# Kernel tuning notes

Hardware: AMD Instinct MI355X
Metric: run time of the kernel (lower is better)

Reference implementation:

```python
import jax, jax.numpy as jnp
import numpy as np

# RoIAlign 2D config (matches init_kwargs)
OUT_H, OUT_W = 7, 7
SPATIAL_SCALE = 0.25
S = 2  # sampling_ratio: S x S sample points per output bin
N, C, H, W = 4, 256, 200, 200
R = 512


def setup_inputs() -> dict:
    key = jax.random.key(0)
    k1, k2, k3, k4, k5 = jax.random.split(key, 5)
    features = jax.random.normal(k1, (N, C, H, W), dtype=jnp.float32)
    # rois in image coordinates (image is H/scale = 800 px): (batch_idx, x1, y1, x2, y2)
    img = H / SPATIAL_SCALE
    b = jax.random.randint(k2, (R,), 0, N).astype(jnp.float32)
    xy1 = jax.random.uniform(k3, (R, 2), dtype=jnp.float32, maxval=img - 96.0)
    wh = jax.random.uniform(k4, (R, 2), dtype=jnp.float32, minval=16.0, maxval=96.0)
    rois = jnp.concatenate([b[:, None], xy1, xy1 + wh], axis=1)  # [R,5]
    return {"features": features, "rois": rois}


def _axis_weights(start, bin_size, out_size, limit):
    """Per-axis sample coords -> (low/high indices [R,out*S,2], lerp weights [R,out*S,2]).
    Matches mmdet/torchvision RoIAlign CUDA kernel semantics."""
    # sample coordinate: start + (i + 0.5) * bin / S  ==  start + ph*bin + (iy+0.5)*bin/S
    i = (jnp.arange(out_size * S, dtype=jnp.float32) + 0.5) / S
    y = start[:, None] + i[None, :] * bin_size[:, None]          # [R, out*S]
    valid = (y >= -1.0) & (y <= limit)                            # kernel: skip if y<-1 or y>H
    yc = jnp.clip(y, 0.0, limit - 1.0)
    yl = jnp.floor(yc).astype(jnp.int32)                          # in [0, H-1]
    yh = jnp.minimum(yl + 1, limit - 1)
    l = yc - yl.astype(jnp.float32)                               # 0 at the top edge, as in kernel
    w = jnp.stack([1.0 - l, l], axis=-1) * valid[..., None].astype(jnp.float32)  # [R,out*S,2]
    idx = jnp.stack([yl, yh], axis=-1)                            # [R,out*S,2]
    return idx, w


def reference(features, rois):
    # order=1 (bilinear) path of RoIAlign2DFunction
    b = rois[:, 0].astype(jnp.int32)                              # [R]
    x1, y1, x2, y2 = (rois[:, k] * SPATIAL_SCALE for k in (1, 2, 3, 4))
    roi_w = jnp.maximum(x2 - x1, 1.0)
    roi_h = jnp.maximum(y2 - y1, 1.0)
    bin_w = roi_w / OUT_W
    bin_h = roi_h / OUT_H

    yidx, wy = _axis_weights(y1, bin_h, OUT_H, H)                 # [R,Hs,2]
    xidx, wx = _axis_weights(x1, bin_w, OUT_W, W)                 # [R,Ws,2]

    nhwc = jnp.transpose(features, (0, 2, 3, 1))                  # [N,H,W,C]
    # gather 2x2 bilinear neighbors for every sample point: [R,Hs,Ws,2,2,C]
    vals = nhwc[b[:, None, None, None, None],
                yidx[:, :, None, :, None],
                xidx[:, None, :, None, :]]
    samples = jnp.einsum('rhwabc,rha,rwb->rhwc', vals, wy, wx)    # [R,Hs,Ws,C]
    Hs, Ws = OUT_H * S, OUT_W * S
    pooled = samples.reshape(R, OUT_H, S, OUT_W, S, C).mean(axis=(2, 4))  # avg over S*S points
    return jnp.transpose(pooled, (0, 3, 1, 2))                    # [R,C,out_h,out_w]
```

## Files before the change

### kernel.cpp

```cpp
#include <hip/hip_runtime.h>


#define OH 7
#define OW 7
#define NSAMP 14
#define NB 4
#define CH 256
#define FH 200
#define FW 200
#define NR 512
#define CCH 16
#define NCHUNK (CH / CCH)
#define PAD 17
#define MAXF 27
#define BLK 256

__global__ __launch_bounds__(BLK) void roialign_fwd(
    const float* __restrict__ feat,
    const float* __restrict__ rois,
    float* __restrict__ out)
{
    __shared__ float tile[MAXF * MAXF * PAD];
    __shared__ int   s_il[2][NSAMP];
    __shared__ int   s_ih[2][NSAMP];
    __shared__ float s_w0[2][NSAMP];
    __shared__ float s_w1[2][NSAMP];

    const int block = blockIdx.x;
    const int r     = block >> 4;
    const int chunk = block & (NCHUNK - 1);
    const int c0    = chunk * CCH;
    const int tid   = threadIdx.x;

    const int   b  = (int)rois[r * 5 + 0];
    const float x1 = rois[r * 5 + 1] * 0.25f;
    const float y1 = rois[r * 5 + 2] * 0.25f;
    const float x2 = rois[r * 5 + 3] * 0.25f;
    const float y2 = rois[r * 5 + 4] * 0.25f;
    const float roi_w = fmaxf(x2 - x1, 1.0f);
    const float roi_h = fmaxf(y2 - y1, 1.0f);
    const float bw = roi_w * (1.0f / OW);
    const float bh = roi_h * (1.0f / OH);

    if (tid < 2 * NSAMP) {
        const int axis = tid >= NSAMP;
        const int i    = tid - axis * NSAMP;
        const float start = axis ? x1 : y1;
        const float bsz   = axis ? bw : bh;
        const float pos   = start + (i + 0.5f) * 0.5f * bsz;
        const float valid = (pos >= -1.0f && pos <= 200.0f) ? 1.0f : 0.0f;
        const float pc    = fminf(fmaxf(pos, 0.0f), 199.0f);
        const int   il    = (int)floorf(pc);
        const int   ih    = min(il + 1, 199);
        const float l     = pc - (float)il;
        s_il[axis][i] = il;
        s_ih[axis][i] = ih;
        s_w0[axis][i] = (1.0f - l) * valid;
        s_w1[axis][i] = l * valid;
    }
    __syncthreads();

    const int ylo = s_il[0][0];
    const int xlo = s_il[1][0];
    int fh = s_ih[0][NSAMP - 1] - ylo + 1;
    int fw = s_ih[1][NSAMP - 1] - xlo + 1;
    fh = min(fh, MAXF);
    fw = min(fw, MAXF);

    {
        const int tx = tid & 31;
        const int ty = tid >> 5;
        const float* fbase =
            feat + ((size_t)(b * CH + c0) * FH + ylo) * FW + xlo;
        for (int y = ty; y < fh; y += BLK / 32) {
            for (int x = tx; x < fw; x += 32) {
                const float* g = fbase + y * FW + x;
                float* l = tile + (y * fw + x) * PAD;
                #pragma unroll
                for (int c = 0; c < CCH; c++) {
                    l[c] = g[(size_t)c * (FH * FW)];
                }
            }
        }
    }
    __syncthreads();

    const int cl   = tid & (CCH - 1);
    const int slot = tid >> 4;
    const float* tc = tile + cl;

    for (int bin = slot; bin < OH * OW; bin += BLK / CCH) {
        const int ph = bin / OW;
        const int pw = bin - ph * OW;
        float acc = 0.0f;
        #pragma unroll
        for (int sy = 0; sy < 2; sy++) {
            const int gy = ph * 2 + sy;
            const int rowl = (s_il[0][gy] - ylo) * fw;
            const int rowh = (s_ih[0][gy] - ylo) * fw;
            const float wy0 = s_w0[0][gy];
            const float wy1 = s_w1[0][gy];
            #pragma unroll
            for (int sx = 0; sx < 2; sx++) {
                const int gx = pw * 2 + sx;
                const int ixl = s_il[1][gx] - xlo;
                const int ixh = s_ih[1][gx] - xlo;
                const float wx0 = s_w0[1][gx];
                const float wx1 = s_w1[1][gx];
                const float v00 = tc[(rowl + ixl) * PAD];
                const float v01 = tc[(rowl + ixh) * PAD];
                const float v10 = tc[(rowh + ixl) * PAD];
                const float v11 = tc[(rowh + ixh) * PAD];
                acc += wy0 * (wx0 * v00 + wx1 * v01)
                     + wy1 * (wx0 * v10 + wx1 * v11);
            }
        }
        out[(size_t)(r * CH + c0 + cl) * (OH * OW) + bin] = acc * 0.25f;
    }
}

extern "C" void kernel_launch(void* const* d_in, const int* in_sizes, int n_in,
                              void* d_out, int out_size, void* d_ws, size_t ws_size,
                              hipStream_t stream) {
    const float* feat = (const float*)d_in[0];
    const float* rois = (const float*)d_in[1];
    float* out = (float*)d_out;
    roialign_fwd<<<NR * NCHUNK, BLK, 0, stream>>>(feat, rois, out);
}
```

Baseline: 251.5 us.

## Switch shared tile to channel-planar layout and halve channel chunk size

Changes the shared-memory tile from a pixel-major layout with padded channel interleave to one plane per channel. It halves the channels per block from 16 to 8, so there are twice as many blocks and each uses less LDS, which should raise occupancy. The load now assigns 16-lane groups to rows of a single channel, so global reads are contiguous along x. The risk is more total blocks and redundant ROI setup per block, and MAXF is lowered to 26, which may clip large ROIs.

```diff
diff --git a/kernel.cpp b/kernel.cpp
--- a/kernel.cpp
+++ b/kernel.cpp
@@ -4,15 +4,14 @@
 #define OH 7
 #define OW 7
 #define NSAMP 14
-#define NB 4
 #define CH 256
 #define FH 200
 #define FW 200
 #define NR 512
-#define CCH 16
+#define CCH 8
 #define NCHUNK (CH / CCH)
-#define PAD 17
-#define MAXF 27
+#define MAXF 26
+#define FPAD (MAXF * MAXF)
 #define BLK 256
 
 __global__ __launch_bounds__(BLK) void roialign_fwd(
@@ -20,14 +19,14 @@
     const float* __restrict__ rois,
     float* __restrict__ out)
 {
-    __shared__ float tile[MAXF * MAXF * PAD];
+    __shared__ float tile[CCH * FPAD];
     __shared__ int   s_il[2][NSAMP];
     __shared__ int   s_ih[2][NSAMP];
     __shared__ float s_w0[2][NSAMP];
     __shared__ float s_w1[2][NSAMP];
 
     const int block = blockIdx.x;
-    const int r     = block >> 4;
+    const int r     = block >> 5;
     const int chunk = block & (NCHUNK - 1);
     const int c0    = chunk * CCH;
     const int tid   = threadIdx.x;
@@ -68,26 +67,25 @@
     fw = min(fw, MAXF);
 
     {
-        const int tx = tid & 31;
-        const int ty = tid >> 5;
+        const int lane = tid & 15;
+        const int gid  = tid >> 4;
+        const int c    = gid & (CCH - 1);
+        const int yb   = gid >> 3;
         const float* fbase =
-            feat + ((size_t)(b * CH + c0) * FH + ylo) * FW + xlo;
-        for (int y = ty; y < fh; y += BLK / 32) {
-            for (int x = tx; x < fw; x += 32) {
-                const float* g = fbase + y * FW + x;
-                float* l = tile + (y * fw + x) * PAD;
-                #pragma unroll
-                for (int c = 0; c < CCH; c++) {
-                    l[c] = g[(size_t)c * (FH * FW)];
-                }
-            }
+            feat + ((size_t)(b * CH + c0 + c) * FH + ylo) * FW + xlo;
+        float* lbase = tile + c * FPAD;
+        for (int y = yb; y < fh; y += 2) {
+            const float* g = fbase + y * FW;
+            float* l = lbase + y * fw;
+            for (int x = lane; x < fw; x += 16)
+                l[x] = g[x];
         }
     }
     __syncthreads();
 
     const int cl   = tid & (CCH - 1);
-    const int slot = tid >> 4;
-    const float* tc = tile + cl;
+    const int slot = tid >> 3;
+    const float* tc = tile + cl * FPAD;
 
     for (int bin = slot; bin < OH * OW; bin += BLK / CCH) {
         const int ph = bin / OW;
@@ -107,12 +105,8 @@
                 const int ixh = s_ih[1][gx] - xlo;
                 const float wx0 = s_w0[1][gx];
                 const float wx1 = s_w1[1][gx];
-                const float v00 = tc[(rowl + ixl) * PAD];
-                const float v01 = tc[(rowl + ixh) * PAD];
-                const float v10 = tc[(rowh + ixl) * PAD];
-                const float v11 = tc[(rowh + ixh) * PAD];
-                acc += wy0 * (wx0 * v00 + wx1 * v01)
-                     + wy1 * (wx0 * v10 + wx1 * v11);
+                acc += wy0 * (wx0 * tc[rowl + ixl] + wx1 * tc[rowl + ixh])
+                     + wy1 * (wx0 * tc[rowh + ixl] + wx1 * tc[rowh + ixh]);
             }
         }
         out[(size_t)(r * CH + c0 + cl) * (OH * OW) + bin] = acc * 0.25f;
```

New measurement: 262.0 us. +4.1%, slower.
